# Kernel optimization log

Hardware: AMD Instinct MI355X
Metric: run time of the kernel (lower is better)

Reference implementation:

```python
import jax, jax.numpy as jnp
import numpy as np

N = 120000   # nodes
E = 1200000  # edges
F_IN = 14    # PascalVOC-SP node features
H = 64       # args.hidden
C = 21       # num_classes
EPS = 1e-5


def _glorot(k, shape):
    fan_in = shape[0]
    return jax.random.normal(k, shape, jnp.float32) / np.sqrt(fan_in).astype(np.float32)


def setup_inputs() -> dict:
    key = jax.random.key(0)
    ks = jax.random.split(key, 16)
    inp = {}
    inp['x1'] = jax.random.normal(ks[0], (N, F_IN), jnp.float32)
    inp['edge_index'] = jax.random.randint(ks[1], (2, E), 0, N)
    dims = [(F_IN, H), (H, H), (H, H), (H, H)]
    i = 2
    for l, (din, dout) in enumerate(dims, 1):
        inp[f'Wn{l}'] = _glorot(ks[i], (din, dout)); i += 1
        inp[f'Wr{l}'] = _glorot(ks[i], (din, dout)); i += 1
        inp[f'b{l}'] = jnp.zeros((dout,), jnp.float32)
    for l in (1, 2, 3):
        inp[f'g{l}'] = jnp.ones((H,), jnp.float32)
        inp[f'be{l}'] = jnp.zeros((H,), jnp.float32)
    inp['Wm0'] = _glorot(ks[10], (H, H))
    inp['gm0'] = jnp.ones((H,), jnp.float32)
    inp['bem0'] = jnp.zeros((H,), jnp.float32)
    inp['Wm1'] = _glorot(ks[11], (H, H))
    inp['gm1'] = jnp.ones((H,), jnp.float32)
    inp['bem1'] = jnp.zeros((H,), jnp.float32)
    inp['Wm2'] = _glorot(ks[12], (H, C))
    inp['bm2'] = jnp.zeros((C,), jnp.float32)
    return inp


def _bn(x, g, b):
    # BatchNorm1d forward with batch statistics (train-mode normalization, biased var)
    m = x.mean(axis=0)
    v = x.var(axis=0)
    return (x - m) * jax.lax.rsqrt(v + EPS) * g + b


def _sage(x, src, dst, Wn, Wr, b):
    # PyG SAGEConv (mean aggr): out = mean_neighbors @ Wn + b + x @ Wr
    s = jax.ops.segment_sum(x[src], dst, num_segments=N)        # [N, d]
    cnt = jax.ops.segment_sum(jnp.ones((src.shape[0],), x.dtype), dst, num_segments=N)
    mean = s / jnp.maximum(cnt, 1.0)[:, None]
    return mean @ Wn + b + x @ Wr


def _lrelu(z):
    return jnp.where(z > 0, z, 0.01 * z)


def reference(x1, edge_index, Wn1, Wr1, b1, Wn2, Wr2, b2, Wn3, Wr3, b3, Wn4, Wr4, b4,
              g1, be1, g2, be2, g3, be3, Wm0, gm0, bem0, Wm1, gm1, bem1, Wm2, bm2):
    src, dst = edge_index[0], edge_index[1]
    x = _bn(_lrelu(_sage(x1, src, dst, Wn1, Wr1, b1)), g1, be1)   # conv1 + bano1 (dropout off)
    x = _bn(_lrelu(_sage(x, src, dst, Wn2, Wr2, b2)), g2, be2)    # conv2 + bano2
    x = _bn(jax.nn.relu(_sage(x, src, dst, Wn3, Wr3, b3)), g3, be3)  # conv3 + bano3
    x = _sage(x, src, dst, Wn4, Wr4, b4)                          # conv4
    # mlpRep: Linear(no bias)->BN->ReLU x2, then Linear(bias), no final act
    x = jax.nn.relu(_bn(x @ Wm0, gm0, bem0))
    x = jax.nn.relu(_bn(x @ Wm1, gm1, bem1))
    return x @ Wm2 + bm2
```

## Files before the change

kernel.cpp:

```cpp
#include <hip/hip_runtime.h>

constexpr int NN = 120000;
constexpr int EE = 1200000;
constexpr float EPSV = 1e-5f;
constexpr int NCBLK   = (NN + 127) / 128;
constexpr int NMFMABLK = NN / 64;
constexpr int ASTRIDE = 32;
constexpr int NSLOT = 64;

constexpr int BNODES  = 128;
constexpr int NBUCK   = (NN + BNODES - 1) / BNODES;
constexpr int BSTRIDE = 1536;
constexpr int EPB3    = 4096;
constexpr int NB3     = (EE + EPB3 - 1) / EPB3;
constexpr int NSTATF  = 5*NSLOT*128;

typedef __attribute__((ext_vector_type(8))) short bf8v;
typedef __attribute__((ext_vector_type(4))) float f4v;

__device__ __forceinline__ float bf2f(unsigned short u){
  union { unsigned i; float f; } v; v.i = ((unsigned)u) << 16; return v.f;
}
__device__ __forceinline__ unsigned short f2bf(float f){
  union { float f; unsigned i; } v; v.f = f;
  unsigned u = v.i;
  return (unsigned short)((u + 0x7FFFu + ((u >> 16) & 1u)) >> 16);
}
__device__ __forceinline__ unsigned pack2(float a, float b){
  return (unsigned)f2bf(a) | ((unsigned)f2bf(b) << 16);
}
__device__ __forceinline__ float act_f(float z, int ACT){
  if (ACT == 1) return z > 0.0f ? z : 0.01f*z;
  if (ACT == 2) return fmaxf(z, 0.0f);
  return z;
}
__device__ __forceinline__ void acc8(uint4 u, float& a0, float& a1, float& a2, float& a3,
                                     float& a4, float& a5, float& a6, float& a7){
  a0 += bf2f((unsigned short)(u.x & 0xFFFF)); a1 += bf2f((unsigned short)(u.x >> 16));
  a2 += bf2f((unsigned short)(u.y & 0xFFFF)); a3 += bf2f((unsigned short)(u.y >> 16));
  a4 += bf2f((unsigned short)(u.z & 0xFFFF)); a5 += bf2f((unsigned short)(u.z >> 16));
  a6 += bf2f((unsigned short)(u.w & 0xFFFF)); a7 += bf2f((unsigned short)(u.w >> 16));
}

__global__ __launch_bounds__(512) void k_bucket(const int* __restrict__ src, const int* __restrict__ dst,
                                                int* __restrict__ cursor, unsigned* __restrict__ bucketed,
                                                float* __restrict__ stats,
                                                const float* __restrict__ x, unsigned* __restrict__ xb){
  __shared__ int hist[NBUCK];
  __shared__ int lstart[NBUCK];
  const int tid = threadIdx.x;
  const int e0  = blockIdx.x * EPB3;
  for (int i = blockIdx.x*512 + tid; i < NSTATF; i += NB3*512) stats[i] = 0.0f;
  for (int i = blockIdx.x*512 + tid; i < NN*8; i += NB3*512){
    int n = i >> 3, j = i & 7;
    int c0 = 2*j, c1 = 2*j + 1;
    float f0 = (c0 < 14) ? x[(size_t)n*14 + c0] : 0.0f;
    float f1 = (c1 < 14) ? x[(size_t)n*14 + c1] : 0.0f;
    xb[i] = pack2(f0, f1);
  }
  for (int i = tid; i < NBUCK; i += 512) hist[i] = 0;
  __syncthreads();

  const bool full = (e0 + EPB3 <= EE);
  if (full){
    #pragma unroll 4
    for (int k = 0; k < EPB3/512; k++){
      int d = dst[e0 + k*512 + tid];
      atomicAdd(&hist[d >> 7], 1);
    }
  } else {
    #pragma unroll 1
    for (int k = 0; k < EPB3/512; k++){
      int e = e0 + k*512 + tid;
      if (e < EE){
        int d = dst[e];
        atomicAdd(&hist[d >> 7], 1);
      }
    }
  }
  __syncthreads();
  for (int i = tid; i < NBUCK; i += 512){
    int h = hist[i];
    lstart[i] = (h > 0) ? atomicAdd(&cursor[i], h) : 0;
  }
  __syncthreads();
  for (int i = tid; i < NBUCK; i += 512) hist[i] = 0;
  __syncthreads();
  #pragma unroll 1
  for (int k = 0; k < EPB3/512; k++){
    int e = e0 + k*512 + tid;
    if (e < EE){
      int d = dst[e];
      int s = src[e];
      int b = d >> 7;
      int r = atomicAdd(&hist[b], 1);
      int idx = lstart[b] + r;
      if (idx < BSTRIDE)
        bucketed[(size_t)b*BSTRIDE + idx] = ((unsigned)s << 7) | (unsigned)(d & 127);
    }
  }
}

__global__ __launch_bounds__(256) void k_buildadj(const unsigned* __restrict__ bucketed,
                                                  const int* __restrict__ cursor,
                                                  int* __restrict__ cnt, int* __restrict__ adj,
                                                  float* __restrict__ invdeg){
  __shared__ alignas(16) int ladj[BNODES*ASTRIDE];
  __shared__ int lcnt[BNODES];
  const int tid = threadIdx.x;
  const int b   = blockIdx.x;
  if (tid < BNODES) lcnt[tid] = 0;
  __syncthreads();
  const int tot = min(cursor[b], BSTRIDE);
  const unsigned* rp = bucketed + (size_t)b*BSTRIDE;
  for (int e = tid; e < tot; e += 256){
    unsigned rec = rp[e];
    int d = (int)(rec & 127u);
    int s = (int)(rec >> 7);
    int p = atomicAdd(&lcnt[d], 1);
    if (p < ASTRIDE) ladj[d*ASTRIDE + p] = s;
  }
  __syncthreads();
  int4* ap = (int4*)(adj + (size_t)b*BNODES*ASTRIDE);
  const int4* lp = (const int4*)ladj;
  #pragma unroll
  for (int i = 0; i < (BNODES*ASTRIDE/4)/256; i++)
    ap[i*256 + tid] = lp[i*256 + tid];
  if (tid < BNODES){
    int c = lcnt[tid];
    int n = b*BNODES + tid;
    cnt[n] = c;
    invdeg[n] = (c > 0) ? (1.0f/(float)c) : -1.0f;
  }
}

__global__ __launch_bounds__(256) void k_prep_conv_frag(const float* __restrict__ Wn, const float* __restrict__ Wr,
                                                        const float* __restrict__ b, const float* __restrict__ statSlots,
                                                        const float* __restrict__ g, const float* __restrict__ be,
                                                        unsigned short* __restrict__ frag, float* __restrict__ bias2){
  __shared__ float sc[64], sh[64];
  int t = threadIdx.x;
  if (t < 64){
    float sum = 0.0f, sq = 0.0f;
    #pragma unroll 8
    for (int s = 0; s < NSLOT; s++){
      sum += statSlots[s*128 + t];
      sq  += statSlots[s*128 + 64 + t];
    }
    float m = sum * (1.0f/NN);
    float v = sq * (1.0f/NN) - m*m;
    float a = g[t] * rsqrtf(v + EPSV);
    sc[t] = a; sh[t] = be[t] - m*a;
  }
  __syncthreads();
  if (blockIdx.x == 0 && t < 64){
    float accB = b[t], accN = 0.0f;
    for (int k=0;k<64;k++){
      accB += sh[k]*Wr[k*64+t];
      accN += sh[k]*Wn[k*64+t];
    }
    bias2[t]      = accB;
    bias2[64 + t] = accN;
  }
  {
    int idx = blockIdx.x*256 + t;
    int j    = idx & 7;
    int lane = (idx >> 3) & 63;
    int kk   = (idx >> 9) & 1;
    int ct   = (idx >> 10) & 3;
    int mat  = (idx >> 12) & 1;
    int k    = kk*32 + (lane >> 4)*8 + j;
    int col  = ct*16 + (lane & 15);
    const float* W = mat ? Wr : Wn;
    frag[idx] = f2bf(sc[k] * W[k*64 + col]);
  }
}

__global__ __launch_bounds__(256) void k_prep_lin_frag(const float* __restrict__ W,
                                                       unsigned short* __restrict__ frag,
                                                       float* __restrict__ bias2,
                                                       const float* __restrict__ bnSlots,
                                                       float* __restrict__ bnRed){
  int t = threadIdx.x;
  if (blockIdx.x == 0 && t < 128){
    bias2[t] = 0.0f;
    if (bnSlots){
      float s = 0.0f;
      #pragma unroll 8
      for (int sl = 0; sl < NSLOT; sl++) s += bnSlots[sl*128 + t];
      bnRed[t] = s;
    }
  }
  {
    int idx = blockIdx.x*256 + t;
    int j    = idx & 7;
    int lane = (idx >> 3) & 63;
    int kk   = (idx >> 9) & 1;
    int ct   = (idx >> 10) & 3;
    int k    = kk*32 + (lane >> 4)*8 + j;
    int col  = ct*16 + (lane & 15);
    frag[idx] = f2bf(W[k*64 + col]);
  }
}

__global__ __launch_bounds__(64) void k_prep_aff(const float* __restrict__ st,
                                                 const float* __restrict__ g, const float* __restrict__ be,
                                                 float* __restrict__ aff){
  int t = threadIdx.x;
  float s = 0.0f, q = 0.0f;
  #pragma unroll 8
  for (int sl = 0; sl < NSLOT; sl++){
    s += st[sl*128 + t];
    q += st[sl*128 + 64 + t];
  }
  float m = s*(1.0f/NN);
  float v = q*(1.0f/NN) - m*m;
  float a = g[t]*rsqrtf(v+EPSV);
  aff[t]      = a;
  aff[64 + t] = be[t] - m*a;
}

template<int ACT, bool STATS>
__global__ __launch_bounds__(256, 1) void k_gmfma(const unsigned short* __restrict__ X,
                                                  const int* __restrict__ cnt, const int* __restrict__ adj,
                                                  const float* __restrict__ invdeg,
                                                  const unsigned short* __restrict__ frag,
                                                  const float* __restrict__ bias2,
                                                  unsigned short* __restrict__ out,
                                                  float* __restrict__ statsOut){
  __shared__ unsigned short sMean[64*72];
  __shared__ float sst[512];
  const int tid  = threadIdx.x;
  const int lane = tid & 63;
  const int wv   = tid >> 6;
  const int nb0  = blockIdx.x*64;

  {
    const int q8 = lane & 7;
    const int h8 = lane >> 3;
    #pragma unroll
    for (int t8 = 0; t8 < 2; t8++){
      const int row = wv*16 + h8*2 + t8;
      const int n   = nb0 + row;
      const int d   = min(cnt[n], ASTRIDE);
      const int st  = n*ASTRIDE;
      float a0=0,a1=0,a2=0,a3=0,a4=0,a5=0,a6=0,a7=0;
      int j = 0;
      for (; j + 7 < d; j += 8){
        int4 sa = *(const int4*)(adj + st + j);
        int4 sb = *(const int4*)(adj + st + j + 4);
        uint4 u0 = *(const uint4*)(X + (size_t)sa.x*64 + 8*q8);
        uint4 u1 = *(const uint4*)(X + (size_t)sa.y*64 + 8*q8);
        uint4 u2 = *(const uint4*)(X + (size_t)sa.z*64 + 8*q8);
        uint4 u3 = *(const uint4*)(X + (size_t)sa.w*64 + 8*q8);
        uint4 u4 = *(const uint4*)(X + (size_t)sb.x*64 + 8*q8);
        uint4 u5 = *(const uint4*)(X + (size_t)sb.y*64 + 8*q8);
        uint4 u6 = *(const uint4*)(X + (size_t)sb.z*64 + 8*q8);
        uint4 u7 = *(const uint4*)(X + (size_t)sb.w*64 + 8*q8);
        acc8(u0,a0,a1,a2,a3,a4,a5,a6,a7); acc8(u1,a0,a1,a2,a3,a4,a5,a6,a7);
        acc8(u2,a0,a1,a2,a3,a4,a5,a6,a7); acc8(u3,a0,a1,a2,a3,a4,a5,a6,a7);
        acc8(u4,a0,a1,a2,a3,a4,a5,a6,a7); acc8(u5,a0,a1,a2,a3,a4,a5,a6,a7);
        acc8(u6,a0,a1,a2,a3,a4,a5,a6,a7); acc8(u7,a0,a1,a2,a3,a4,a5,a6,a7);
      }
      for (; j + 3 < d; j += 4){
        int4 sa = *(const int4*)(adj + st + j);
        uint4 u0 = *(const uint4*)(X + (size_t)sa.x*64 + 8*q8);
        uint4 u1 = *(const uint4*)(X + (size_t)sa.y*64 + 8*q8);
        uint4 u2 = *(const uint4*)(X + (size_t)sa.z*64 + 8*q8);
        uint4 u3 = *(const uint4*)(X + (size_t)sa.w*64 + 8*q8);
        acc8(u0,a0,a1,a2,a3,a4,a5,a6,a7); acc8(u1,a0,a1,a2,a3,a4,a5,a6,a7);
        acc8(u2,a0,a1,a2,a3,a4,a5,a6,a7); acc8(u3,a0,a1,a2,a3,a4,a5,a6,a7);
      }
      for (; j < d; j++){
        int s = adj[st + j];
        uint4 u = *(const uint4*)(X + (size_t)s*64 + 8*q8);
        acc8(u,a0,a1,a2,a3,a4,a5,a6,a7);
      }
      float iv = fmaxf(invdeg[n], 0.0f);
      uint4 o;
      o.x = pack2(a0*iv, a1*iv);
      o.y = pack2(a2*iv, a3*iv);
      o.z = pack2(a4*iv, a5*iv);
      o.w = pack2(a6*iv, a7*iv);
      *(uint4*)(sMean + row*72 + 8*q8) = o;
    }
  }

  const bf8v* fp = (const bf8v*)frag;
  bf8v wn[4][2], wr[4][2];
  #pragma unroll
  for (int ct=0;ct<4;ct++){
    #pragma unroll
    for (int kk=0;kk<2;kk++){
      wn[ct][kk] = fp[((0*4+ct)*2+kk)*64 + lane];
      wr[ct][kk] = fp[((1*4+ct)*2+kk)*64 + lane];
    }
  }
  const int m  = lane & 15;
  const int kq = lane >> 4;
  const size_t arow = (size_t)(nb0 + wv*16 + m)*64;
  bf8v ax0 = *(const bf8v*)(X + arow + kq*8);
  bf8v ax1 = *(const bf8v*)(X + arow + 32 + kq*8);
  __syncthreads();
  bf8v am0 = *(const bf8v*)(sMean + (wv*16 + m)*72 + kq*8);
  bf8v am1 = *(const bf8v*)(sMean + (wv*16 + m)*72 + 32 + kq*8);

  f4v acc[4];
  #pragma unroll
  for (int ct=0;ct<4;ct++){
    f4v c = {0.0f,0.0f,0.0f,0.0f};
    c = __builtin_amdgcn_mfma_f32_16x16x32_bf16(am0, wn[ct][0], c, 0,0,0);
    c = __builtin_amdgcn_mfma_f32_16x16x32_bf16(am1, wn[ct][1], c, 0,0,0);
    c = __builtin_amdgcn_mfma_f32_16x16x32_bf16(ax0, wr[ct][0], c, 0,0,0);
    c = __builtin_amdgcn_mfma_f32_16x16x32_bf16(ax1, wr[ct][1], c, 0,0,0);
    acc[ct] = c;
  }

  const int col = lane & 15;
  float bb[4], bg[4];
  #pragma unroll
  for (int ct=0;ct<4;ct++){
    bb[ct] = bias2[ct*16 + col];
    bg[ct] = bias2[64 + ct*16 + col];
  }
  float ls[4] = {0,0,0,0}, lq[4] = {0,0,0,0};
  #pragma unroll
  for (int r=0;r<4;r++){
    const int node = nb0 + wv*16 + (lane>>4)*4 + r;
    float gadd = (invdeg[node] > 0.0f) ? 1.0f : 0.0f;
    #pragma unroll
    for (int ct=0;ct<4;ct++){
      float z = acc[ct][r] + bb[ct] + gadd * bg[ct];
      z = act_f(z, ACT);
      out[(size_t)node*64 + ct*16 + col] = f2bf(z);
      if (STATS){ ls[ct] += z; lq[ct] = fmaf(z, z, lq[ct]); }
    }
  }
  if constexpr (STATS){
    #pragma unroll
    for (int ct=0;ct<4;ct++){
      float s = ls[ct]; s += __shfl_down(s, 32); s += __shfl_down(s, 16);
      float q = lq[ct]; q += __shfl_down(q, 32); q += __shfl_down(q, 16);
      if (kq == 0){
        sst[wv*128 + ct*16 + col]      = s;
        sst[wv*128 + 64 + ct*16 + col] = q;
      }
    }
    __syncthreads();
    if (tid < 128){
      float v = sst[tid] + sst[128+tid] + sst[256+tid] + sst[384+tid];
      atomicAdd(&statsOut[(blockIdx.x & (NSLOT-1))*128 + tid], v);
    }
  }
}

template<int ACT, bool STATS, bool BNA>
__global__ __launch_bounds__(256, 1) void k_mfma_lin(const unsigned short* __restrict__ Ax,
                                                     const unsigned short* __restrict__ frag,
                                                     const float* __restrict__ bias2,
                                                     unsigned short* __restrict__ out,
                                                     float* __restrict__ statsOut,
                                                     const float* __restrict__ bnRed,
                                                     const float* __restrict__ bnG,
                                                     const float* __restrict__ bnB){
  __shared__ float sst[512];
  const int lane = threadIdx.x & 63;
  const int wv   = threadIdx.x >> 6;
  const int n0   = (blockIdx.x*4 + wv)*16;
  const int m    = lane & 15;
  const int kq   = lane >> 4;

  const bf8v* fp = (const bf8v*)frag;
  bf8v wr[4][2];
  #pragma unroll
  for (int ct=0;ct<4;ct++){
    #pragma unroll
    for (int kk=0;kk<2;kk++) wr[ct][kk] = fp[(ct*2+kk)*64 + lane];
  }

  const size_t arow = (size_t)(n0 + m)*64;
  bf8v ax0 = *(const bf8v*)(Ax + arow + kq*8);
  bf8v ax1 = *(const bf8v*)(Ax + arow + 32 + kq*8);
  if constexpr (BNA){
    #pragma unroll
    for (int j=0;j<8;j++){
      int k0 = kq*8 + j, k1 = 32 + kq*8 + j;
      float m0 = bnRed[k0]*(1.0f/NN);
      float v0 = bnRed[64+k0]*(1.0f/NN) - m0*m0;
      float a0 = bnG[k0]*rsqrtf(v0+EPSV);
      float b0 = bnB[k0] - m0*a0;
      ax0[j] = (short)f2bf(fmaxf(fmaf(a0, bf2f((unsigned short)ax0[j]), b0), 0.0f));
      float m1 = bnRed[k1]*(1.0f/NN);
      float v1 = bnRed[64+k1]*(1.0f/NN) - m1*m1;
      float a1 = bnG[k1]*rsqrtf(v1+EPSV);
      float b1 = bnB[k1] - m1*a1;
      ax1[j] = (short)f2bf(fmaxf(fmaf(a1, bf2f((unsigned short)ax1[j]), b1), 0.0f));
    }
  }

  f4v acc[4];
  #pragma unroll
  for (int ct=0;ct<4;ct++){
    f4v c = {0.0f,0.0f,0.0f,0.0f};
    c = __builtin_amdgcn_mfma_f32_16x16x32_bf16(ax0, wr[ct][0], c, 0,0,0);
    c = __builtin_amdgcn_mfma_f32_16x16x32_bf16(ax1, wr[ct][1], c, 0,0,0);
    acc[ct] = c;
  }

  const int col = lane & 15;
  float bb[4];
  #pragma unroll
  for (int ct=0;ct<4;ct++) bb[ct] = bias2[ct*16 + col];
  float ls[4] = {0,0,0,0}, lq[4] = {0,0,0,0};
  #pragma unroll
  for (int r=0;r<4;r++){
    const int node = n0 + (lane>>4)*4 + r;
    #pragma unroll
    for (int ct=0;ct<4;ct++){
      float z = act_f(acc[ct][r] + bb[ct], ACT);
      out[(size_t)node*64 + ct*16 + col] = f2bf(z);
      if (STATS){ ls[ct] += z; lq[ct] = fmaf(z, z, lq[ct]); }
    }
  }
  if constexpr (STATS){
    #pragma unroll
    for (int ct=0;ct<4;ct++){
      float s = ls[ct]; s += __shfl_down(s, 32); s += __shfl_down(s, 16);
      float q = lq[ct]; q += __shfl_down(q, 32); q += __shfl_down(q, 16);
      if (kq == 0){
        sst[wv*128 + ct*16 + col]      = s;
        sst[wv*128 + 64 + ct*16 + col] = q;
      }
    }
    __syncthreads();
    if (threadIdx.x < 128){
      float v = sst[threadIdx.x] + sst[128+threadIdx.x] + sst[256+threadIdx.x] + sst[384+threadIdx.x];
      atomicAdd(&statsOut[(blockIdx.x & (NSLOT-1))*128 + threadIdx.x], v);
    }
  }
}

__global__ __launch_bounds__(128, 1) void k_conv1(const unsigned* __restrict__ xb, const float* __restrict__ x,
                                                  const int* __restrict__ cnt, const int* __restrict__ adj,
                                                  const float* __restrict__ invdeg,
                                                  const float* __restrict__ Wn, const float* __restrict__ Wr,
                                                  const float* __restrict__ b,
                                                  unsigned short* __restrict__ out, float* __restrict__ statsOut){
  constexpr int DIN = 14, RS = 15;
  __shared__ float sMean[128*RS];
  __shared__ float sX[128*RS];
  const int tid = threadIdx.x;
  const int lane = tid & 63;
  const int n0  = blockIdx.x*128;
  const int n   = n0 + tid;
  const bool valid = (n < NN);

  {
    const float* gp = x + (size_t)n0*DIN;
    for (int i = tid; i < 128*DIN; i += 128){
      int r = i / DIN, c = i - r*DIN;
      sX[r*RS + c] = (n0 + r < NN) ? gp[i] : 0.0f;
    }
  }

  {
    float mm[14];
    #pragma unroll
    for (int j=0;j<14;j++) mm[j] = 0.0f;
    const int d  = valid ? min(cnt[n], ASTRIDE) : 0;
    const int st = n*ASTRIDE;
    #pragma unroll 2
    for (int j=0;j<d;j++){
      int s = adj[st+j];
      const uint4* rp = (const uint4*)(xb + s*8);
      uint4 u0 = rp[0], u1 = rp[1];
      mm[0]+=bf2f((unsigned short)(u0.x&0xFFFF)); mm[1]+=bf2f((unsigned short)(u0.x>>16));
      mm[2]+=bf2f((unsigned short)(u0.y&0xFFFF)); mm[3]+=bf2f((unsigned short)(u0.y>>16));
      mm[4]+=bf2f((unsigned short)(u0.z&0xFFFF)); mm[5]+=bf2f((unsigned short)(u0.z>>16));
      mm[6]+=bf2f((unsigned short)(u0.w&0xFFFF)); mm[7]+=bf2f((unsigned short)(u0.w>>16));
      mm[8]+=bf2f((unsigned short)(u1.x&0xFFFF)); mm[9]+=bf2f((unsigned short)(u1.x>>16));
      mm[10]+=bf2f((unsigned short)(u1.y&0xFFFF)); mm[11]+=bf2f((unsigned short)(u1.y>>16));
      mm[12]+=bf2f((unsigned short)(u1.z&0xFFFF)); mm[13]+=bf2f((unsigned short)(u1.z>>16));
    }
    float iv = valid ? invdeg[n] : -1.0f;
    float gate = (iv > 0.0f) ? iv : 0.0f;
    #pragma unroll
    for (int j=0;j<14;j++) sMean[tid*RS + j] = mm[j]*gate;
  }
  __syncthreads();

  float accA0[32], accA1[32];
  #pragma unroll
  for (int jj=0;jj<32;jj++){ accA0[jj]=0.0f; accA1[jj]=0.0f; }

  #pragma unroll 1
  for (int k=0;k<DIN;k++){
    float rv = sMean[tid*RS + k];
    const float* wr = Wn + k*64;
    #pragma unroll
    for (int jj=0;jj<32;jj++) accA0[jj] = fmaf(wr[jj],    rv, accA0[jj]);
    #pragma unroll
    for (int jj=0;jj<32;jj++) accA1[jj] = fmaf(wr[32+jj], rv, accA1[jj]);
  }
  #pragma unroll 1
  for (int k=0;k<DIN;k++){
    float rv = sX[tid*RS + k];
    const float* wr = Wr + k*64;
    #pragma unroll
    for (int jj=0;jj<32;jj++) accA0[jj] = fmaf(wr[jj],    rv, accA0[jj]);
    #pragma unroll
    for (int jj=0;jj<32;jj++) accA1[jj] = fmaf(wr[32+jj], rv, accA1[jj]);
  }

  uint2* o2 = (uint2*)(out + (size_t)n*64);
  float vs[64], vq[64];
  #pragma unroll
  for (int q=0;q<8;q++){
    float z0 = valid ? act_f(accA0[4*q+0]+b[4*q+0],1) : 0.0f;
    float z1 = valid ? act_f(accA0[4*q+1]+b[4*q+1],1) : 0.0f;
    float z2 = valid ? act_f(accA0[4*q+2]+b[4*q+2],1) : 0.0f;
    float z3 = valid ? act_f(accA0[4*q+3]+b[4*q+3],1) : 0.0f;
    vs[4*q+0] = z0; vs[4*q+1] = z1; vs[4*q+2] = z2; vs[4*q+3] = z3;
    if (valid){ uint2 t; t.x = pack2(z0,z1); t.y = pack2(z2,z3); o2[q] = t; }
  }
  #pragma unroll
  for (int q=0;q<8;q++){
    float z0 = valid ? act_f(accA1[4*q+0]+b[32+4*q+0],1) : 0.0f;
    float z1 = valid ? act_f(accA1[4*q+1]+b[32+4*q+1],1) : 0.0f;
    float z2 = valid ? act_f(accA1[4*q+2]+b[32+4*q+2],1) : 0.0f;
    float z3 = valid ? act_f(accA1[4*q+3]+b[32+4*q+3],1) : 0.0f;
    vs[32+4*q+0] = z0; vs[32+4*q+1] = z1; vs[32+4*q+2] = z2; vs[32+4*q+3] = z3;
    if (valid){ uint2 t; t.x = pack2(z0,z1); t.y = pack2(z2,z3); o2[8+q] = t; }
  }
  #pragma unroll
  for (int j=0;j<64;j++) vq[j] = vs[j]*vs[j];

  #pragma unroll
  for (int k=0;k<6;k++){
    const bool keep1 = ((lane >> k) & 1) != 0;
    const int half = 64 >> (k+1);
    #pragma unroll
    for (int i=0;i<half;i++){
      float sa = vs[2*i], sb = vs[2*i+1];
      float qa = vq[2*i], qb = vq[2*i+1];
      float skeep = keep1 ? sb : sa;
      float ssend = keep1 ? sa : sb;
      float qkeep = keep1 ? qb : qa;
      float qsend = keep1 ? qa : qb;
      vs[i] = skeep + __shfl_xor(ssend, 1<<k);
      vq[i] = qkeep + __shfl_xor(qsend, 1<<k);
    }
  }
  const int slot = (blockIdx.x & (NSLOT-1))*128;
  atomicAdd(&statsOut[slot + lane],      vs[0]);
  atomicAdd(&statsOut[slot + 64 + lane], vq[0]);
}

__global__ __launch_bounds__(256, 1) void k_lin21(const unsigned short* __restrict__ x,
                                                  const float* __restrict__ W, const float* __restrict__ bias,
                                                  const float* __restrict__ aff,
                                                  float* __restrict__ out){
  __shared__ float sW[64*21];
  __shared__ float sAff[128];
  const int tid = threadIdx.x;
  if (tid < 128) sAff[tid] = aff[tid];
  for (int i = tid; i < 64*21; i += 256) sW[i] = W[i];
  __syncthreads();

  const int p  = tid & 3;
  const int nl = tid >> 2;
  const int n  = blockIdx.x*64 + nl;
  const bool valid = (n < NN);
  const int k0 = p*16;

  uint4 u0 = {0,0,0,0}, u1 = {0,0,0,0};
  if (valid){
    const unsigned short* rp = x + (size_t)n*64 + k0;
    u0 = *(const uint4*)(rp);
    u1 = *(const uint4*)(rp + 8);
  }
  float f[16];
  f[0]=bf2f((unsigned short)(u0.x&0xFFFF)); f[1]=bf2f((unsigned short)(u0.x>>16));
  f[2]=bf2f((unsigned short)(u0.y&0xFFFF)); f[3]=bf2f((unsigned short)(u0.y>>16));
  f[4]=bf2f((unsigned short)(u0.z&0xFFFF)); f[5]=bf2f((unsigned short)(u0.z>>16));
  f[6]=bf2f((unsigned short)(u0.w&0xFFFF)); f[7]=bf2f((unsigned short)(u0.w>>16));
  f[8]=bf2f((unsigned short)(u1.x&0xFFFF)); f[9]=bf2f((unsigned short)(u1.x>>16));
  f[10]=bf2f((unsigned short)(u1.y&0xFFFF)); f[11]=bf2f((unsigned short)(u1.y>>16));
  f[12]=bf2f((unsigned short)(u1.z&0xFFFF)); f[13]=bf2f((unsigned short)(u1.z>>16));
  f[14]=bf2f((unsigned short)(u1.w&0xFFFF)); f[15]=bf2f((unsigned short)(u1.w>>16));
  #pragma unroll
  for (int j=0;j<16;j++)
    f[j] = fmaxf(fmaf(sAff[k0+j], f[j], sAff[64+k0+j]), 0.0f);

  float a[21];
  #pragma unroll
  for (int jj=0;jj<21;jj++) a[jj] = 0.0f;
  #pragma unroll
  for (int k=0;k<16;k++){
    const float* wr = sW + (k0+k)*21;
    float rv = f[k];
    #pragma unroll
    for (int jj=0;jj<21;jj++) a[jj] = fmaf(wr[jj], rv, a[jj]);
  }
  #pragma unroll
  for (int jj=0;jj<21;jj++){
    a[jj] += __shfl_xor(a[jj], 1);
    a[jj] += __shfl_xor(a[jj], 2);
  }
  if (valid){
    const int c0 = p*6;
    const int ce = (p == 3) ? 21 : c0 + 6;
    float* op = out + (size_t)n*21;
    #pragma unroll 6
    for (int jj=c0; jj<ce; jj++) op[jj] = a[jj] + bias[jj];
  }
}

extern "C" void kernel_launch(void* const* d_in, const int* in_sizes, int n_in,
                              void* d_out, int out_size, void* d_ws, size_t ws_size,
                              hipStream_t stream){
  const float* x1  = (const float*)d_in[0];
  const int*   ei  = (const int*)d_in[1];
  const int* srcp = ei;
  const int* dstp = ei + EE;
  const float *Wn1=(const float*)d_in[2],  *Wr1=(const float*)d_in[3],  *b1=(const float*)d_in[4];
  const float *Wn2=(const float*)d_in[5],  *Wr2=(const float*)d_in[6],  *b2=(const float*)d_in[7];
  const float *Wn3=(const float*)d_in[8],  *Wr3=(const float*)d_in[9],  *b3=(const float*)d_in[10];
  const float *Wn4=(const float*)d_in[11], *Wr4=(const float*)d_in[12], *b4=(const float*)d_in[13];
  const float *g1=(const float*)d_in[14], *be1=(const float*)d_in[15];
  const float *g2=(const float*)d_in[16], *be2=(const float*)d_in[17];
  const float *g3=(const float*)d_in[18], *be3=(const float*)d_in[19];
  const float *Wm0=(const float*)d_in[20], *gm0=(const float*)d_in[21], *bem0=(const float*)d_in[22];
  const float *Wm1=(const float*)d_in[23], *gm1=(const float*)d_in[24], *bem1=(const float*)d_in[25];
  const float *Wm2=(const float*)d_in[26], *bm2=(const float*)d_in[27];
  float* out = (float*)d_out;

  char* ws = (char*)d_ws;
  int*   cnt     = (int*)(ws);
  float* invdeg  = (float*)(ws + (1ull<<20));
  int*   adj     = (int*)(ws + (2ull<<20));
  unsigned short* hA   = (unsigned short*)(ws + (25ull<<20));
  unsigned short* hB   = (unsigned short*)(ws + (41ull<<20));
  float* stats   = (float*)(ws + (57ull<<20));
  float* bnRed   = (float*)(ws + (57ull<<20) + 192*1024);
  float* aff5    = (float*)(ws + (57ull<<20) + 224*1024);
  unsigned short* fragC = (unsigned short*)(ws + (58ull<<20));
  float* bias2C  = (float*)(ws + (58ull<<20) + 65536);
  unsigned short* fragL = (unsigned short*)(ws + (59ull<<20));
  float* bias2L  = (float*)(ws + (59ull<<20) + 65536);
  unsigned* xb   = (unsigned*)(ws + (60ull<<20));
  unsigned* bucketed = (unsigned*)(ws + (25ull<<20));
  int* cursor        = (int*)(ws + (25ull<<20) + (6ull<<20));

  float* S1 = stats;
  float* S2 = stats + NSLOT*128;
  float* S3 = stats + 2*NSLOT*128;
  float* S4 = stats + 3*NSLOT*128;
  float* S5 = stats + 4*NSLOT*128;

  hipMemsetAsync(cursor, 0, NBUCK*sizeof(int), stream);
  k_bucket  <<<NB3,  512,0,stream>>>(srcp, dstp, cursor, bucketed, stats, x1, xb);
  k_buildadj<<<NBUCK,256,0,stream>>>(bucketed, cursor, cnt, adj, invdeg);

  k_conv1<<<NCBLK,128,0,stream>>>(xb,x1,cnt,adj,invdeg,Wn1,Wr1,b1,hA,S1);

  k_prep_conv_frag<<<32,256,0,stream>>>(Wn2,Wr2,b2,S1,g1,be1,fragC,bias2C);
  k_gmfma<1,true><<<NMFMABLK,256,0,stream>>>(hA,cnt,adj,invdeg,fragC,bias2C,hB,S2);

  k_prep_conv_frag<<<32,256,0,stream>>>(Wn3,Wr3,b3,S2,g2,be2,fragC,bias2C);
  k_gmfma<2,true><<<NMFMABLK,256,0,stream>>>(hB,cnt,adj,invdeg,fragC,bias2C,hA,S3);

  k_prep_conv_frag<<<32,256,0,stream>>>(Wn4,Wr4,b4,S3,g3,be3,fragC,bias2C);
  k_gmfma<0,false><<<NMFMABLK,256,0,stream>>>(hA,cnt,adj,invdeg,fragC,bias2C,hB,nullptr);

  k_prep_lin_frag<<<16,256,0,stream>>>(Wm0, fragL, bias2L, nullptr, nullptr);
  k_mfma_lin<0,true,false><<<NMFMABLK,256,0,stream>>>(hB,fragL,bias2L,hA,S4,nullptr,nullptr,nullptr);

  k_prep_lin_frag<<<16,256,0,stream>>>(Wm1, fragL, bias2L, S4, bnRed);
  k_mfma_lin<0,true,true><<<NMFMABLK,256,0,stream>>>(hA,fragL,bias2L,hB,S5,bnRed,gm0,bem0);

  k_prep_aff<<<1,64,0,stream>>>(S5, gm1, bem1, aff5);
  k_lin21<<<NMFMABLK,256,0,stream>>>(hB,Wm2,bm2,aff5,out);
}
```

Measured before the change: 362.4 us.

## Split conv1 work across four threads per node with 512-thread blocks

Conv1 moves from one thread per node to four threads per node. Each thread gathers a strided quarter of the neighbours, the partial sums are combined with xor shuffles, and each thread computes and stores 16 of the 64 output columns. The stats reduction now goes through shared memory across 8 waves before the atomics. The aim is to cut per-thread register pressure (64 accumulators down to 16) and raise memory-level parallelism in the gather, at the cost of extra shuffles and a block-wide sync.

```diff
diff --git a/kernel.cpp b/kernel.cpp
--- a/kernel.cpp
+++ b/kernel.cpp
@@ -440,7 +440,7 @@
   }
 }
 
-__global__ __launch_bounds__(128, 1) void k_conv1(const unsigned* __restrict__ xb, const float* __restrict__ x,
+__global__ __launch_bounds__(512, 1) void k_conv1(const unsigned* __restrict__ xb, const float* __restrict__ x,
                                                   const int* __restrict__ cnt, const int* __restrict__ adj,
                                                   const float* __restrict__ invdeg,
                                                   const float* __restrict__ Wn, const float* __restrict__ Wr,
@@ -449,15 +449,20 @@
   constexpr int DIN = 14, RS = 15;
   __shared__ float sMean[128*RS];
   __shared__ float sX[128*RS];
-  const int tid = threadIdx.x;
+  __shared__ float sst[8*128];
+  const int tid  = threadIdx.x;
   const int lane = tid & 63;
-  const int n0  = blockIdx.x*128;
-  const int n   = n0 + tid;
+  const int wv   = tid >> 6;
+  const int p    = tid & 3;
+  const int nl   = tid >> 2;
+  const int n0   = blockIdx.x*128;
+  const int n    = n0 + nl;
   const bool valid = (n < NN);
+  const int c0   = p*16;
 
   {
     const float* gp = x + (size_t)n0*DIN;
-    for (int i = tid; i < 128*DIN; i += 128){
+    for (int i = tid; i < 128*DIN; i += 512){
       int r = i / DIN, c = i - r*DIN;
       sX[r*RS + c] = (n0 + r < NN) ? gp[i] : 0.0f;
     }
@@ -469,8 +474,7 @@
     for (int j=0;j<14;j++) mm[j] = 0.0f;
     const int d  = valid ? min(cnt[n], ASTRIDE) : 0;
     const int st = n*ASTRIDE;
-    #pragma unroll 2
-    for (int j=0;j<d;j++){
+    for (int j=p; j<d; j+=4){
       int s = adj[st+j];
       const uint4* rp = (const uint4*)(xb + s*8);
       uint4 u0 = rp[0], u1 = rp[1];
@@ -482,63 +486,58 @@
       mm[10]+=bf2f((unsigned short)(u1.y&0xFFFF)); mm[11]+=bf2f((unsigned short)(u1.y>>16));
       mm[12]+=bf2f((unsigned short)(u1.z&0xFFFF)); mm[13]+=bf2f((unsigned short)(u1.z>>16));
     }
+    #pragma unroll
+    for (int j=0;j<14;j++){
+      mm[j] += __shfl_xor(mm[j], 1);
+      mm[j] += __shfl_xor(mm[j], 2);
+    }
     float iv = valid ? invdeg[n] : -1.0f;
     float gate = (iv > 0.0f) ? iv : 0.0f;
-    #pragma unroll
-    for (int j=0;j<14;j++) sMean[tid*RS + j] = mm[j]*gate;
-  }
-  __syncthreads();
-
-  float accA0[32], accA1[32];
-  #pragma unroll
-  for (int jj=0;jj<32;jj++){ accA0[jj]=0.0f; accA1[jj]=0.0f; }
-
+    if (p == 0){
+      #pragma unroll
+      for (int j=0;j<14;j++) sMean[nl*RS + j] = mm[j]*gate;
+    }
+  }
+  __syncthreads();
+
+  float acc[16];
+  #pragma unroll
+  for (int jj=0;jj<16;jj++) acc[jj] = 0.0f;
   #pragma unroll 1
   for (int k=0;k<DIN;k++){
-    float rv = sMean[tid*RS + k];
-    const float* wr = Wn + k*64;
-    #pragma unroll
-    for (int jj=0;jj<32;jj++) accA0[jj] = fmaf(wr[jj],    rv, accA0[jj]);
-    #pragma unroll
-    for (int jj=0;jj<32;jj++) accA1[jj] = fmaf(wr[32+jj], rv, accA1[jj]);
+    float rv = sMean[nl*RS + k];
+    const float* wr = Wn + k*64 + c0;
+    #pragma unroll
+    for (int jj=0;jj<16;jj++) acc[jj] = fmaf(wr[jj], rv, acc[jj]);
   }
   #pragma unroll 1
   for (int k=0;k<DIN;k++){
-    float rv = sX[tid*RS + k];
-    const float* wr = Wr + k*64;
-    #pragma unroll
-    for (int jj=0;jj<32;jj++) accA0[jj] = fmaf(wr[jj],    rv, accA0[jj]);
-    #pragma unroll
-    for (int jj=0;jj<32;jj++) accA1[jj] = fmaf(wr[32+jj], rv, accA1[jj]);
-  }
-
-  uint2* o2 = (uint2*)(out + (size_t)n*64);
-  float vs[64], vq[64];
-  #pragma unroll
-  for (int q=0;q<8;q++){
-    float z0 = valid ? act_f(accA0[4*q+0]+b[4*q+0],1) : 0.0f;
-    float z1 = valid ? act_f(accA0[4*q+1]+b[4*q+1],1) : 0.0f;
-    float z2 = valid ? act_f(accA0[4*q+2]+b[4*q+2],1) : 0.0f;
-    float z3 = valid ? act_f(accA0[4*q+3]+b[4*q+3],1) : 0.0f;
-    vs[4*q+0] = z0; vs[4*q+1] = z1; vs[4*q+2] = z2; vs[4*q+3] = z3;
-    if (valid){ uint2 t; t.x = pack2(z0,z1); t.y = pack2(z2,z3); o2[q] = t; }
-  }
-  #pragma unroll
-  for (int q=0;q<8;q++){
-    float z0 = valid ? act_f(accA1[4*q+0]+b[32+4*q+0],1) : 0.0f;
-    float z1 = valid ? act_f(accA1[4*q+1]+b[32+4*q+1],1) : 0.0f;
-    float z2 = valid ? act_f(accA1[4*q+2]+b[32+4*q+2],1) : 0.0f;
-    float z3 = valid ? act_f(accA1[4*q+3]+b[32+4*q+3],1) : 0.0f;
-    vs[32+4*q+0] = z0; vs[32+4*q+1] = z1; vs[32+4*q+2] = z2; vs[32+4*q+3] = z3;
-    if (valid){ uint2 t; t.x = pack2(z0,z1); t.y = pack2(z2,z3); o2[8+q] = t; }
-  }
-  #pragma unroll
-  for (int j=0;j<64;j++) vq[j] = vs[j]*vs[j];
-
-  #pragma unroll
-  for (int k=0;k<6;k++){
-    const bool keep1 = ((lane >> k) & 1) != 0;
-    const int half = 64 >> (k+1);
+    float rv = sX[nl*RS + k];
+    const float* wr = Wr + k*64 + c0;
+    #pragma unroll
+    for (int jj=0;jj<16;jj++) acc[jj] = fmaf(wr[jj], rv, acc[jj]);
+  }
+
+  float vs[16], vq[16];
+  #pragma unroll
+  for (int q=0;q<16;q++){
+    float z = valid ? act_f(acc[q] + b[c0+q], 1) : 0.0f;
+    vs[q] = z; vq[q] = z*z;
+  }
+  if (valid){
+    uint4 t0, t1;
+    t0.x = pack2(vs[0],vs[1]);   t0.y = pack2(vs[2],vs[3]);
+    t0.z = pack2(vs[4],vs[5]);   t0.w = pack2(vs[6],vs[7]);
+    t1.x = pack2(vs[8],vs[9]);   t1.y = pack2(vs[10],vs[11]);
+    t1.z = pack2(vs[12],vs[13]); t1.w = pack2(vs[14],vs[15]);
+    uint4* op = (uint4*)(out + (size_t)n*64 + c0);
+    op[0] = t0; op[1] = t1;
+  }
+
+  #pragma unroll
+  for (int k=0;k<4;k++){
+    const bool keep1 = ((lane >> (k+2)) & 1) != 0;
+    const int half = 16 >> (k+1);
     #pragma unroll
     for (int i=0;i<half;i++){
       float sa = vs[2*i], sb = vs[2*i+1];
@@ -547,13 +546,20 @@
       float ssend = keep1 ? sa : sb;
       float qkeep = keep1 ? qb : qa;
       float qsend = keep1 ? qa : qb;
-      vs[i] = skeep + __shfl_xor(ssend, 1<<k);
-      vq[i] = qkeep + __shfl_xor(qsend, 1<<k);
-    }
-  }
-  const int slot = (blockIdx.x & (NSLOT-1))*128;
-  atomicAdd(&statsOut[slot + lane],      vs[0]);
-  atomicAdd(&statsOut[slot + 64 + lane], vq[0]);
+      vs[i] = skeep + __shfl_xor(ssend, 4<<k);
+      vq[i] = qkeep + __shfl_xor(qsend, 4<<k);
+    }
+  }
+  const int f = c0 + (lane>>2);
+  sst[wv*128 + f]      = vs[0];
+  sst[wv*128 + 64 + f] = vq[0];
+  __syncthreads();
+  if (tid < 128){
+    float v = 0.0f;
+    #pragma unroll
+    for (int w=0;w<8;w++) v += sst[w*128 + tid];
+    atomicAdd(&statsOut[(blockIdx.x & (NSLOT-1))*128 + tid], v);
+  }
 }
 
 __global__ __launch_bounds__(256, 1) void k_lin21(const unsigned short* __restrict__ x,
@@ -662,7 +668,7 @@
   k_bucket  <<<NB3,  512,0,stream>>>(srcp, dstp, cursor, bucketed, stats, x1, xb);
   k_buildadj<<<NBUCK,256,0,stream>>>(bucketed, cursor, cnt, adj, invdeg);
 
-  k_conv1<<<NCBLK,128,0,stream>>>(xb,x1,cnt,adj,invdeg,Wn1,Wr1,b1,hA,S1);
+  k_conv1<<<NCBLK,512,0,stream>>>(xb,x1,cnt,adj,invdeg,Wn1,Wr1,b1,hA,S1);
 
   k_prep_conv_frag<<<32,256,0,stream>>>(Wn2,Wr2,b2,S1,g1,be1,fragC,bias2C);
   k_gmfma<1,true><<<NMFMABLK,256,0,stream>>>(hA,cnt,adj,invdeg,fragC,bias2C,hB,S2);
```

Measured after the change: 397.6 us. 9.7% more time.
